# Optimization experiments

Measured on AMD Instinct MI355X. Metric: run time of the kernel, lower is better.

## Reference

```python
import jax, jax.numpy as jnp
import numpy as np

N, E, B = 20000, 160000, 64
NFEAT, NHID, HEADS, NCLASS = 128, 64, 16, 10
GAT_SLOPE = 0.2    # LeakyReLU inside GATv2 attention
OUT_SLOPE = 0.01   # torch.nn.functional.leaky_relu default
TEMPERATURE = 1.0


def _lrelu(x, slope):
    return jnp.where(x >= 0, x, slope * x)


def gatv2_conv(x, src, dst, Wl, bl, Wr, br, att, bias):
    # x: [N, Fin]; PyG GATv2Conv with share_weights=False, concat=False (mean over heads)
    xl = (x @ Wl + bl).reshape(N, HEADS, NHID)   # source-side transform
    xr = (x @ Wr + br).reshape(N, HEADS, NHID)   # target-side transform
    e = _lrelu(xl[src] + xr[dst], GAT_SLOPE)     # [E', H, C] per-edge pre-activation
    logit = jnp.einsum('ehc,hc->eh', e, att)     # [E', H]
    # segment softmax over incoming edges of each target node (self-loops guarantee >=1 edge)
    m = jax.ops.segment_max(logit, dst, num_segments=N)
    m = jnp.where(jnp.isfinite(m), m, 0.0)
    ex = jnp.exp(logit - m[dst])
    den = jax.ops.segment_sum(ex, dst, num_segments=N)
    alpha = ex / den[dst]                        # [E', H]
    out = jax.ops.segment_sum(alpha[:, :, None] * xl[src], dst, num_segments=N)  # [N, H, C]
    return out.mean(axis=1) + bias               # concat=False -> head average, then bias


def setup_inputs() -> dict:
    key = jax.random.key(0)
    ks = jax.random.split(key, 20)
    s = 0.05
    inp = {
        'x': jax.random.normal(ks[0], (N, NFEAT), dtype=jnp.float32),
        'edge_index': jax.random.randint(ks[1], (2, E), 0, N, dtype=jnp.int64)
            if jax.config.jax_enable_x64 else jax.random.randint(ks[1], (2, E), 0, N).astype(jnp.int32),
        'batch': jnp.sort(jax.random.randint(ks[2], (N,), 0, B)).astype(jnp.int32),
        # GATv2 layer 1
        'W1l': jax.random.normal(ks[3], (NFEAT, HEADS * NHID), dtype=jnp.float32) * s,
        'b1l': jnp.zeros((HEADS * NHID,), jnp.float32),
        'W1r': jax.random.normal(ks[4], (NFEAT, HEADS * NHID), dtype=jnp.float32) * s,
        'b1r': jnp.zeros((HEADS * NHID,), jnp.float32),
        'att1': jax.random.normal(ks[5], (HEADS, NHID), dtype=jnp.float32) * s,
        'bias1': jnp.zeros((NHID,), jnp.float32),
        # GATv2 layer 2
        'W2l': jax.random.normal(ks[6], (NHID, HEADS * NHID), dtype=jnp.float32) * s,
        'b2l': jnp.zeros((HEADS * NHID,), jnp.float32),
        'W2r': jax.random.normal(ks[7], (NHID, HEADS * NHID), dtype=jnp.float32) * s,
        'b2r': jnp.zeros((HEADS * NHID,), jnp.float32),
        'att2': jax.random.normal(ks[8], (HEADS, NHID), dtype=jnp.float32) * s,
        'bias2': jnp.zeros((NHID,), jnp.float32),
        # heads
        'Wc': jax.random.normal(ks[9], (NHID, NCLASS), dtype=jnp.float32) * s,
        'bc': jnp.zeros((NCLASS,), jnp.float32),
        'Wv': jax.random.normal(ks[10], (NHID, 1), dtype=jnp.float32) * s,
        'bv': jnp.zeros((1,), jnp.float32),
    }
    return inp


def reference(x, edge_index, batch, W1l, b1l, W1r, b1r, att1, bias1,
              W2l, b2l, W2r, b2r, att2, bias2, Wc, bc, Wv, bv):
    loop = jnp.arange(N, dtype=edge_index.dtype)  # PyG add_self_loops=True
    src = jnp.concatenate([edge_index[0], loop])
    dst = jnp.concatenate([edge_index[1], loop])

    h = _lrelu(gatv2_conv(x, src, dst, W1l, b1l, W1r, b1r, att1, bias1), OUT_SLOPE)
    h = _lrelu(gatv2_conv(h, src, dst, W2l, b2l, W2r, b2r, att2, bias2), OUT_SLOPE)
    # dropout p=0.0 -> identity

    sums = jax.ops.segment_sum(h, batch, num_segments=B)           # [B, NHID]
    cnt = jax.ops.segment_sum(jnp.ones((N,), h.dtype), batch, num_segments=B)
    pooled = sums / jnp.maximum(cnt, 1.0)[:, None]                 # global_mean_pool

    logits = (pooled @ Wc + bc) / TEMPERATURE                      # [B, NCLASS]
    log_var = pooled @ Wv + bv                                     # [B, 1]
    return (logits, log_var)
```

## Files before the change

kernel.cpp:

```cpp
#include <hip/hip_runtime.h>
#include <hip/hip_bf16.h>
#include <hip/hip_fp16.h>
#include <math.h>

#define NN   20000
#define EE   160000
#define NBAT 64
#define NF   128
#define NH   64
#define NHEAD 16
#define NCLS 10
#define ETOT (EE + NN)

typedef __attribute__((ext_vector_type(8))) short short8;
typedef __attribute__((ext_vector_type(8))) _Float16 half8;
typedef __attribute__((ext_vector_type(2))) _Float16 h2v;
typedef __attribute__((ext_vector_type(4))) float f32x4;
typedef unsigned short ushort_t;

#if __has_builtin(__builtin_amdgcn_fdot2)
typedef __fp16 fdot2_t __attribute__((ext_vector_type(2)));
static __device__ __forceinline__ float dot2(h2v a, h2v b, float c) {
    return __builtin_amdgcn_fdot2(__builtin_bit_cast(fdot2_t, a),
                                  __builtin_bit_cast(fdot2_t, b), c, false);
}
#else
static __device__ __forceinline__ float dot2(h2v a, h2v b, float c) {
    return c + (float)a.x * (float)b.x + (float)a.y * (float)b.y;
}
#endif

static __device__ __forceinline__ ushort_t f2bf_rn(float x) {
    unsigned u = __builtin_bit_cast(unsigned, x);
    unsigned r = (u + 0x7fffu + ((u >> 16) & 1u)) >> 16;
    return (ushort_t)r;
}
static __device__ __forceinline__ float bf2f(ushort_t u) {
    unsigned v = (unsigned)u << 16;
    return __builtin_bit_cast(float, v);
}

__global__ void k_hist(const int* __restrict__ ei, int* __restrict__ deg) {
    int e = blockIdx.x * 256 + threadIdx.x;
    if (e < EE) atomicAdd(&deg[ei[EE + e]], 1);
}

__global__ void k_scan(const int* __restrict__ deg, int* __restrict__ rowptr,
                       int* __restrict__ cursor, int* __restrict__ csr) {
    const int T = 1024, PER = (NN + T - 1) / T;
    __shared__ int part[T];
    int t = threadIdx.x;
    int local[PER];
    int s = 0;
    #pragma unroll
    for (int i = 0; i < PER; ++i) {
        int idx = t * PER + i;
        int v = (idx < NN) ? deg[idx] : 0;
        local[i] = v; s += v;
    }
    part[t] = s;
    __syncthreads();
    for (int off = 1; off < T; off <<= 1) {
        int v = (t >= off) ? part[t - off] : 0;
        __syncthreads();
        part[t] += v;
        __syncthreads();
    }
    int ex = (t == 0) ? 0 : part[t - 1];
    #pragma unroll
    for (int i = 0; i < PER; ++i) {
        int idx = t * PER + i;
        if (idx < NN) {
            int base = ex + idx;
            rowptr[idx] = base;
            csr[base]   = idx;
            cursor[idx] = base + 1;
            ex += local[i];
        }
    }
    if (t == T - 1) rowptr[NN] = ex + NN;
}

__global__ void k_scatter(const int* __restrict__ ei, int* __restrict__ cursor,
                          int* __restrict__ csr) {
    int e = blockIdx.x * 256 + threadIdx.x;
    if (e >= EE) return;
    int s = ei[e], d = ei[EE + e];
    int pos = atomicAdd(&cursor[d], 1);
    csr[pos] = s;
}

__global__ void k_bounds(const int* __restrict__ batch, int* __restrict__ bstart) {
    int n = blockIdx.x * 256 + threadIdx.x;
    if (n >= NN) return;
    int b = batch[n];
    if (n == 0) for (int bb = 0; bb <= b; ++bb) bstart[bb] = 0;
    int bn = (n + 1 < NN) ? batch[n + 1] : NBAT;
    for (int bb = b + 1; bb <= bn; ++bb) bstart[bb] = n + 1;
}

__global__ void k_split_w4(
    const float* __restrict__ W0, ushort_t* __restrict__ h0, ushort_t* __restrict__ l0,
    const float* __restrict__ W1, ushort_t* __restrict__ h1, ushort_t* __restrict__ l1,
    const float* __restrict__ W2, ushort_t* __restrict__ h2p, ushort_t* __restrict__ l2,
    const float* __restrict__ W3, ushort_t* __restrict__ h3, ushort_t* __restrict__ l3)
{
    const int z = blockIdx.y;
    const float* W; ushort_t* hi; ushort_t* lo; int K;
    if      (z == 0) { W = W0; hi = h0;  lo = l0; K = NF; }
    else if (z == 1) { W = W1; hi = h1;  lo = l1; K = NF; }
    else if (z == 2) { W = W2; hi = h2p; lo = l2; K = NH; }
    else             { W = W3; hi = h3;  lo = l3; K = NH; }
    int idx = blockIdx.x * 256 + threadIdx.x;
    if (idx >= K * 1024) return;
    int k = idx >> 10, n = idx & 1023;
    float x = W[idx];
    ushort_t h = f2bf_rn(x);
    hi[n * K + k] = h;
    lo[n * K + k] = f2bf_rn(x - bf2f(h));
}


template<int K>
__global__ __launch_bounds__(256) void k_gemm_l1(
    const float* __restrict__ X, int M,
    const ushort_t* __restrict__ W0hi, const ushort_t* __restrict__ W0lo,
    const float* __restrict__ b0, _Float16* __restrict__ O0,
    const ushort_t* __restrict__ W1hi, const ushort_t* __restrict__ W1lo,
    const float* __restrict__ b1, _Float16* __restrict__ O1)
{
    const ushort_t* Whi = blockIdx.z ? W1hi : W0hi;
    const ushort_t* Wlo = blockIdx.z ? W1lo : W0lo;
    const float*    bi  = blockIdx.z ? b1 : b0;
    _Float16*       O   = blockIdx.z ? O1 : O0;

    const int r0 = blockIdx.x * 128;
    const int c0 = blockIdx.y * 128;

    __shared__ __align__(16) ushort_t As_hi[128 * 64];
    __shared__ __align__(16) ushort_t As_lo[128 * 64];
    __shared__ __align__(16) ushort_t Ws_hi[128 * 64];
    __shared__ __align__(16) ushort_t Ws_lo[128 * 64];

    const int t = threadIdx.x;
    const int lane = t & 63;
    const int wv = t >> 6, wr = wv >> 1, wc = wv & 1;
    const int fr = lane & 15;
    const int k0 = (lane >> 4) * 8;

    f32x4 acc[4][4] = {};

    for (int kt = 0; kt < K; kt += 64) {
        #pragma unroll
        for (int p = 0; p < 4; ++p) {
            int idx = p * 256 + t;
            int m  = idx >> 3;
            int kc = (idx & 7) * 8;
            int gr = r0 + m;
            uint4 H = make_uint4(0, 0, 0, 0), L = make_uint4(0, 0, 0, 0);
            if (gr < M) {
                float4 v0 = *(const float4*)(X + (size_t)gr * K + kt + kc);
                float4 v1 = *(const float4*)(X + (size_t)gr * K + kt + kc + 4);
                float vv[8] = {v0.x, v0.y, v0.z, v0.w, v1.x, v1.y, v1.z, v1.w};
                unsigned hh[8], ll[8];
                #pragma unroll
                for (int q = 0; q < 8; ++q) {
                    hh[q] = f2bf_rn(vv[q]);
                    ll[q] = f2bf_rn(vv[q] - bf2f((ushort_t)hh[q]));
                }
                H = make_uint4(hh[0] | (hh[1] << 16), hh[2] | (hh[3] << 16),
                               hh[4] | (hh[5] << 16), hh[6] | (hh[7] << 16));
                L = make_uint4(ll[0] | (ll[1] << 16), ll[2] | (ll[3] << 16),
                               ll[4] | (ll[5] << 16), ll[6] | (ll[7] << 16));
            }
            int sw = (m * 128 + kc * 2) ^ ((m & 7) << 4);
            *(uint4*)((char*)As_hi + sw) = H;
            *(uint4*)((char*)As_lo + sw) = L;
            uint4 wh = *(const uint4*)(Whi + (size_t)(c0 + m) * K + kt + kc);
            uint4 wl = *(const uint4*)(Wlo + (size_t)(c0 + m) * K + kt + kc);
            *(uint4*)((char*)Ws_hi + sw) = wh;
            *(uint4*)((char*)Ws_lo + sw) = wl;
        }
        __syncthreads();

        #pragma unroll
        for (int ks = 0; ks < 64; ks += 32) {
            short8 ah[4], al[4], bh[4], bl[4];
            #pragma unroll
            for (int i = 0; i < 4; ++i) {
                int row = wr * 64 + i * 16 + fr;
                int off = (row * 128 + (ks + k0) * 2) ^ ((row & 7) << 4);
                ah[i] = *(const short8*)((const char*)As_hi + off);
                al[i] = *(const short8*)((const char*)As_lo + off);
            }
            #pragma unroll
            for (int j = 0; j < 4; ++j) {
                int col = wc * 64 + j * 16 + fr;
                int off = (col * 128 + (ks + k0) * 2) ^ ((col & 7) << 4);
                bh[j] = *(const short8*)((const char*)Ws_hi + off);
                bl[j] = *(const short8*)((const char*)Ws_lo + off);
            }
            #pragma unroll
            for (int i = 0; i < 4; ++i)
                #pragma unroll
                for (int j = 0; j < 4; ++j) {
                    acc[i][j] = __builtin_amdgcn_mfma_f32_16x16x32_bf16(ah[i], bh[j], acc[i][j], 0, 0, 0);
                    acc[i][j] = __builtin_amdgcn_mfma_f32_16x16x32_bf16(ah[i], bl[j], acc[i][j], 0, 0, 0);
                    acc[i][j] = __builtin_amdgcn_mfma_f32_16x16x32_bf16(al[i], bh[j], acc[i][j], 0, 0, 0);
                }
        }
        __syncthreads();
    }

    float bj[4];
    #pragma unroll
    for (int j = 0; j < 4; ++j) bj[j] = bi[c0 + wc * 64 + j * 16 + fr];
    #pragma unroll
    for (int i = 0; i < 4; ++i) {
        int rbase = r0 + wr * 64 + i * 16 + (lane >> 4) * 4;
        #pragma unroll
        for (int r = 0; r < 4; ++r) {
            int gr = rbase + r;
            if (gr < M) {
                #pragma unroll
                for (int j = 0; j < 4; ++j)
                    O[(size_t)gr * 1024 + c0 + wc * 64 + j * 16 + fr] =
                        (_Float16)(acc[i][j][r] + bj[j]);
            }
        }
    }
}

template<int K>
__global__ __launch_bounds__(256) void k_gemm_mfma(
    const ushort_t* __restrict__ Ahi, const ushort_t* __restrict__ Alo, int M,
    const ushort_t* __restrict__ W0hi, const ushort_t* __restrict__ W0lo,
    const float* __restrict__ b0, _Float16* __restrict__ O0,
    const ushort_t* __restrict__ W1hi, const ushort_t* __restrict__ W1lo,
    const float* __restrict__ b1, _Float16* __restrict__ O1)
{
    const ushort_t* Whi = blockIdx.z ? W1hi : W0hi;
    const ushort_t* Wlo = blockIdx.z ? W1lo : W0lo;
    const float*    bi  = blockIdx.z ? b1 : b0;
    _Float16*       O   = blockIdx.z ? O1 : O0;

    const int r0 = blockIdx.x * 128;
    const int c0 = blockIdx.y * 128;

    __shared__ __align__(16) ushort_t As_hi[128 * 64];
    __shared__ __align__(16) ushort_t As_lo[128 * 64];
    __shared__ __align__(16) ushort_t Ws_hi[128 * 64];
    __shared__ __align__(16) ushort_t Ws_lo[128 * 64];

    const int t = threadIdx.x;
    const int lane = t & 63;
    const int wv = t >> 6, wr = wv >> 1, wc = wv & 1;
    const int fr = lane & 15;
    const int k0 = (lane >> 4) * 8;

    f32x4 acc[4][4] = {};

    for (int kt = 0; kt < K; kt += 64) {
        #pragma unroll
        for (int p = 0; p < 4; ++p) {
            int idx = p * 256 + t;
            int m  = idx >> 3;
            int kc = (idx & 7) * 8;
            int gr = r0 + m;
            uint4 vh = make_uint4(0, 0, 0, 0), vl = make_uint4(0, 0, 0, 0);
            if (gr < M) {
                vh = *(const uint4*)(Ahi + (size_t)gr * K + kt + kc);
                vl = *(const uint4*)(Alo + (size_t)gr * K + kt + kc);
            }
            int sw = (m * 128 + kc * 2) ^ ((m & 7) << 4);
            *(uint4*)((char*)As_hi + sw) = vh;
            *(uint4*)((char*)As_lo + sw) = vl;
            uint4 wh = *(const uint4*)(Whi + (size_t)(c0 + m) * K + kt + kc);
            uint4 wl = *(const uint4*)(Wlo + (size_t)(c0 + m) * K + kt + kc);
            *(uint4*)((char*)Ws_hi + sw) = wh;
            *(uint4*)((char*)Ws_lo + sw) = wl;
        }
        __syncthreads();

        #pragma unroll
        for (int ks = 0; ks < 64; ks += 32) {
            short8 ah[4], al[4], bh[4], bl[4];
            #pragma unroll
            for (int i = 0; i < 4; ++i) {
                int row = wr * 64 + i * 16 + fr;
                int off = (row * 128 + (ks + k0) * 2) ^ ((row & 7) << 4);
                ah[i] = *(const short8*)((const char*)As_hi + off);
                al[i] = *(const short8*)((const char*)As_lo + off);
            }
            #pragma unroll
            for (int j = 0; j < 4; ++j) {
                int col = wc * 64 + j * 16 + fr;
                int off = (col * 128 + (ks + k0) * 2) ^ ((col & 7) << 4);
                bh[j] = *(const short8*)((const char*)Ws_hi + off);
                bl[j] = *(const short8*)((const char*)Ws_lo + off);
            }
            #pragma unroll
            for (int i = 0; i < 4; ++i)
                #pragma unroll
                for (int j = 0; j < 4; ++j) {
                    acc[i][j] = __builtin_amdgcn_mfma_f32_16x16x32_bf16(ah[i], bh[j], acc[i][j], 0, 0, 0);
                    acc[i][j] = __builtin_amdgcn_mfma_f32_16x16x32_bf16(ah[i], bl[j], acc[i][j], 0, 0, 0);
                    acc[i][j] = __builtin_amdgcn_mfma_f32_16x16x32_bf16(al[i], bh[j], acc[i][j], 0, 0, 0);
                }
        }
        __syncthreads();
    }

    float bj[4];
    #pragma unroll
    for (int j = 0; j < 4; ++j) bj[j] = bi[c0 + wc * 64 + j * 16 + fr];
    #pragma unroll
    for (int i = 0; i < 4; ++i) {
        int rbase = r0 + wr * 64 + i * 16 + (lane >> 4) * 4;
        #pragma unroll
        for (int r = 0; r < 4; ++r) {
            int gr = rbase + r;
            if (gr < M) {
                #pragma unroll
                for (int j = 0; j < 4; ++j)
                    O[(size_t)gr * 1024 + c0 + wc * 64 + j * 16 + fr] =
                        (_Float16)(acc[i][j][r] + bj[j]);
            }
        }
    }
}

static __device__ __forceinline__ float logit8(
    half8 a0, half8 a1, half8 xr0, half8 xr1, const h2v* att2)
{
    half8 t0 = a0 + xr0;
    half8 t1 = a1 + xr1;
    t0 = __builtin_elementwise_max(t0, t0 * (_Float16)0.2f);
    t1 = __builtin_elementwise_max(t1, t1 * (_Float16)0.2f);
    const h2v* p0 = (const h2v*)&t0;
    const h2v* p1 = (const h2v*)&t1;
    float lg = 0.f;
    #pragma unroll
    for (int j = 0; j < 4; ++j) lg = dot2(p0[j], att2[j], lg);
    #pragma unroll
    for (int j = 0; j < 4; ++j) lg = dot2(p1[j], att2[4 + j], lg);
    return lg;
}

template<int SPLIT>
__global__ __launch_bounds__(256) void k_attn(
    const _Float16* __restrict__ xl, const _Float16* __restrict__ xr,
    const float* __restrict__ att, const float* __restrict__ bias,
    const int* __restrict__ rowptr, const int* __restrict__ csr,
    float* __restrict__ hout, ushort_t* __restrict__ hhi, ushort_t* __restrict__ hlo)
{
    const int wave = threadIdx.x >> 6;
    const int lane = threadIdx.x & 63;
    const int n = blockIdx.x * 4 + wave;
    if (n >= NN) return;
    const int h  = lane >> 2;
    const int cc = lane & 3;
    const int cb = h * NH + cc * 16;

    h2v att2[8];
    #pragma unroll
    for (int i = 0; i < 4; ++i) {
        float4 a = *(const float4*)(att + cb + i * 4);
        att2[i * 2 + 0] = h2v{(_Float16)a.x, (_Float16)a.y};
        att2[i * 2 + 1] = h2v{(_Float16)a.z, (_Float16)a.w};
    }
    const half8 xr0 = *(const half8*)(xr + (size_t)n * 1024 + cb);
    const half8 xr1 = *(const half8*)(xr + (size_t)n * 1024 + cb + 8);

    float acc[16];
    #pragma unroll
    for (int j = 0; j < 16; ++j) acc[j] = 0.f;
    float den = 0.f;

    const int e0 = rowptr[n], e1 = rowptr[n + 1];
    for (int e = e0; e < e1; e += 4) {
        int src[4];
        #pragma unroll
        for (int j = 0; j < 4; ++j) {
            int ee = e + j;
            src[j] = csr[(ee < e1) ? ee : (e1 - 1)];
        }
        half8 xa0[4], xa1[4];
        #pragma unroll
        for (int j = 0; j < 4; ++j) {
            const _Float16* p = xl + (size_t)src[j] * 1024 + cb;
            xa0[j] = *(const half8*)p;
            xa1[j] = *(const half8*)(p + 8);
        }
        #pragma unroll
        for (int j = 0; j < 4; ++j) {
            float lg = logit8(xa0[j], xa1[j], xr0, xr1, att2);
            lg += __shfl_xor(lg, 1);
            lg += __shfl_xor(lg, 2);
            float p = (e + j < e1) ? __expf(lg) : 0.f;
            den += p;
            const _Float16* va = (const _Float16*)&xa0[j];
            const _Float16* vb = (const _Float16*)&xa1[j];
            #pragma unroll
            for (int q = 0; q < 8; ++q) acc[q]     = fmaf((float)va[q], p, acc[q]);
            #pragma unroll
            for (int q = 0; q < 8; ++q) acc[8 + q] = fmaf((float)vb[q], p, acc[8 + q]);
        }
    }

    const float inv = 1.f / den;
    float v[16];
    #pragma unroll
    for (int j = 0; j < 16; ++j) v[j] = acc[j] * inv;
    #pragma unroll
    for (int mask = 4; mask <= 32; mask <<= 1)
        #pragma unroll
        for (int j = 0; j < 16; ++j) v[j] += __shfl_xor(v[j], mask);

    if (h == 0) {
        float bvv[16];
        #pragma unroll
        for (int i = 0; i < 4; ++i)
            *(float4*)(bvv + i * 4) = *(const float4*)(bias + cc * 16 + i * 4);
        #pragma unroll
        for (int i = 0; i < 4; ++i) {
            float o[4];
            #pragma unroll
            for (int r = 0; r < 4; ++r) {
                float tt = v[i * 4 + r] * 0.0625f + bvv[i * 4 + r];
                o[r] = fmaxf(tt, 0.01f * tt);
            }
            if (SPLIT) {
                ushort4 hh, ll;
                hh.x = f2bf_rn(o[0]); ll.x = f2bf_rn(o[0] - bf2f(hh.x));
                hh.y = f2bf_rn(o[1]); ll.y = f2bf_rn(o[1] - bf2f(hh.y));
                hh.z = f2bf_rn(o[2]); ll.z = f2bf_rn(o[2] - bf2f(hh.z));
                hh.w = f2bf_rn(o[3]); ll.w = f2bf_rn(o[3] - bf2f(hh.w));
                *(ushort4*)(hhi + (size_t)n * NH + cc * 16 + i * 4) = hh;
                *(ushort4*)(hlo + (size_t)n * NH + cc * 16 + i * 4) = ll;
            } else {
                *(float4*)(hout + (size_t)n * NH + cc * 16 + i * 4) =
                    make_float4(o[0], o[1], o[2], o[3]);
            }
        }
    }
}

#define PNODES 128
__global__ __launch_bounds__(256) void k_pool_partial(
    const float* __restrict__ h2buf, const int* __restrict__ batch,
    float* __restrict__ sums)
{
    const int n0 = blockIdx.x * PNODES;
    const int c = threadIdx.x & 63;
    const int r = threadIdx.x >> 6;
    const int nend = (n0 + PNODES < NN) ? n0 + PNODES : NN;
    float s = 0.f;
    int bcur = -1;
    for (int n = n0 + r; n < nend; n += 4) {
        int b = batch[n];
        if (b != bcur) {
            if (bcur >= 0) atomicAdd(&sums[bcur * NH + c], s);
            bcur = b; s = 0.f;
        }
        s += h2buf[(size_t)n * NH + c];
    }
    if (bcur >= 0) atomicAdd(&sums[bcur * NH + c], s);
}

__global__ void k_heads(const float* __restrict__ sums, const int* __restrict__ bstart,
                        const float* __restrict__ Wc, const float* __restrict__ bc,
                        const float* __restrict__ Wv, const float* __restrict__ bv,
                        float* __restrict__ out)
{
    const int b = blockIdx.x, c = threadIdx.x;
    const float cnt = (float)(bstart[b + 1] - bstart[b]);
    const float pooled = sums[b * NH + c] / fmaxf(cnt, 1.f);
    __shared__ float pl[NH];
    pl[c] = pooled;
    __syncthreads();
    if (c < NCLS) {
        float a = bc[c];
        for (int k = 0; k < NH; ++k) a = fmaf(pl[k], Wc[k * NCLS + c], a);
        out[b * NCLS + c] = a;
    } else if (c == NCLS) {
        float a = bv[0];
        for (int k = 0; k < NH; ++k) a = fmaf(pl[k], Wv[k], a);
        out[NBAT * NCLS + b] = a;
    }
}

extern "C" void kernel_launch(void* const* d_in, const int* in_sizes, int n_in,
                              void* d_out, int out_size, void* d_ws, size_t ws_size,
                              hipStream_t stream)
{
    const float* x     = (const float*)d_in[0];
    const int*   ei    = (const int*)  d_in[1];
    const int*   batch = (const int*)  d_in[2];
    const float* W1l = (const float*)d_in[3],  *b1l = (const float*)d_in[4];
    const float* W1r = (const float*)d_in[5],  *b1r = (const float*)d_in[6];
    const float* att1 = (const float*)d_in[7], *bias1 = (const float*)d_in[8];
    const float* W2l = (const float*)d_in[9],  *b2l = (const float*)d_in[10];
    const float* W2r = (const float*)d_in[11], *b2r = (const float*)d_in[12];
    const float* att2 = (const float*)d_in[13], *bias2 = (const float*)d_in[14];
    const float* Wc = (const float*)d_in[15],  *bc = (const float*)d_in[16];
    const float* Wv = (const float*)d_in[17],  *bv = (const float*)d_in[18];
    float* out = (float*)d_out;

    char* ws = (char*)d_ws;
    size_t off = 0;
    auto carve = [&](size_t bytes) {
        char* p = ws + off;
        off = (off + bytes + 255) & ~(size_t)255;
        return p;
    };
    _Float16* xl    = (_Float16*)carve((size_t)NN * 1024 * 2);
    _Float16* xr    = (_Float16*)carve((size_t)NN * 1024 * 2);
    float*    h2b   = (float*)carve((size_t)NN * NH * 4);
    float*    psums = (float*)carve((size_t)NBAT * NH * 4);
    ushort_t* h1hi  = (ushort_t*)carve((size_t)NN * NH * 2);
    ushort_t* h1lo  = (ushort_t*)carve((size_t)NN * NH * 2);
    ushort_t* Wt1lh = (ushort_t*)carve((size_t)1024 * NF * 2);
    ushort_t* Wt1ll = (ushort_t*)carve((size_t)1024 * NF * 2);
    ushort_t* Wt1rh = (ushort_t*)carve((size_t)1024 * NF * 2);
    ushort_t* Wt1rl = (ushort_t*)carve((size_t)1024 * NF * 2);
    ushort_t* Wt2lh = (ushort_t*)carve((size_t)1024 * NH * 2);
    ushort_t* Wt2ll = (ushort_t*)carve((size_t)1024 * NH * 2);
    ushort_t* Wt2rh = (ushort_t*)carve((size_t)1024 * NH * 2);
    ushort_t* Wt2rl = (ushort_t*)carve((size_t)1024 * NH * 2);
    int*      deg    = (int*)carve((size_t)NN * 4);
    int*      cursor = (int*)carve((size_t)NN * 4);
    int*      rowptr = (int*)carve((size_t)(NN + 1) * 4);
    int*      csr    = (int*)carve((size_t)ETOT * 4);
    int*      bstart = (int*)carve((size_t)(NBAT + 1) * 4);

    hipMemsetAsync(deg, 0, (size_t)NN * 4, stream);
    k_hist   <<<(EE + 255) / 256, 256, 0, stream>>>(ei, deg);
    k_scan   <<<1, 1024, 0, stream>>>(deg, rowptr, cursor, csr);
    k_scatter<<<(EE + 255) / 256, 256, 0, stream>>>(ei, cursor, csr);
    k_bounds <<<(NN + 255) / 256, 256, 0, stream>>>(batch, bstart);

    k_split_w4<<<dim3((NF * 1024 + 255) / 256, 4), 256, 0, stream>>>(
        W1l, Wt1lh, Wt1ll, W1r, Wt1rh, Wt1rl,
        W2l, Wt2lh, Wt2ll, W2r, Wt2rh, Wt2rl);

    const int MB = (NN + 127) / 128;
    k_gemm_l1<NF><<<dim3(MB, 8, 2), 256, 0, stream>>>(
        x, NN, Wt1lh, Wt1ll, b1l, xl, Wt1rh, Wt1rl, b1r, xr);
    k_attn<1><<<NN / 4, 256, 0, stream>>>(xl, xr, att1, bias1, rowptr, csr,
                                          (float*)nullptr, h1hi, h1lo);
    k_gemm_mfma<NH><<<dim3(MB, 8, 2), 256, 0, stream>>>(
        h1hi, h1lo, NN, Wt2lh, Wt2ll, b2l, xl, Wt2rh, Wt2rl, b2r, xr);
    k_attn<0><<<NN / 4, 256, 0, stream>>>(xl, xr, att2, bias2, rowptr, csr,
                                          h2b, (ushort_t*)nullptr, (ushort_t*)nullptr);
    hipMemsetAsync(psums, 0, (size_t)NBAT * NH * 4, stream);
    k_pool_partial<<<(NN + PNODES - 1) / PNODES, 256, 0, stream>>>(h2b, batch, psums);
    k_heads<<<NBAT, NH, 0, stream>>>(psums, bstart, Wc, bc, Wv, bv, out);
}
```

Baseline: 386.0 us.

## Replace split-bf16 triple MFMA GEMMs with single fp16 MFMA and staged stores

Drops the hi/lo bf16 split emulation of fp32 in both projection GEMMs, using plain fp16 operands and one f16 MFMA per tile instead of three. This also halves the weight and activation staging traffic and the LDS footprint. Layer-2 input h1 is now stored as fp16, and the layer-2 GEMM loses its K loop since K fits in a single tile. Outputs are staged through swizzled LDS so global writes become coalesced 16-byte stores. The cost is lower precision: fp16 operands have a 10-bit mantissa instead of the near-fp32 accuracy of the split, which may affect tolerance.

```diff
diff --git a/kernel.cpp b/kernel.cpp
--- a/kernel.cpp
+++ b/kernel.cpp
@@ -12,7 +12,6 @@
 #define NCLS 10
 #define ETOT (EE + NN)
 
-typedef __attribute__((ext_vector_type(8))) short short8;
 typedef __attribute__((ext_vector_type(8))) _Float16 half8;
 typedef __attribute__((ext_vector_type(2))) _Float16 h2v;
 typedef __attribute__((ext_vector_type(4))) float f32x4;
@@ -29,16 +28,6 @@
     return c + (float)a.x * (float)b.x + (float)a.y * (float)b.y;
 }
 #endif
-
-static __device__ __forceinline__ ushort_t f2bf_rn(float x) {
-    unsigned u = __builtin_bit_cast(unsigned, x);
-    unsigned r = (u + 0x7fffu + ((u >> 16) & 1u)) >> 16;
-    return (ushort_t)r;
-}
-static __device__ __forceinline__ float bf2f(ushort_t u) {
-    unsigned v = (unsigned)u << 16;
-    return __builtin_bit_cast(float, v);
-}
 
 __global__ void k_hist(const int* __restrict__ ei, int* __restrict__ deg) {
     int e = blockIdx.x * 256 + threadIdx.x;
@@ -100,47 +89,40 @@
 }
 
 __global__ void k_split_w4(
-    const float* __restrict__ W0, ushort_t* __restrict__ h0, ushort_t* __restrict__ l0,
-    const float* __restrict__ W1, ushort_t* __restrict__ h1, ushort_t* __restrict__ l1,
-    const float* __restrict__ W2, ushort_t* __restrict__ h2p, ushort_t* __restrict__ l2,
-    const float* __restrict__ W3, ushort_t* __restrict__ h3, ushort_t* __restrict__ l3)
+    const float* __restrict__ W0, _Float16* __restrict__ T0,
+    const float* __restrict__ W1, _Float16* __restrict__ T1,
+    const float* __restrict__ W2, _Float16* __restrict__ T2,
+    const float* __restrict__ W3, _Float16* __restrict__ T3)
 {
     const int z = blockIdx.y;
-    const float* W; ushort_t* hi; ushort_t* lo; int K;
-    if      (z == 0) { W = W0; hi = h0;  lo = l0; K = NF; }
-    else if (z == 1) { W = W1; hi = h1;  lo = l1; K = NF; }
-    else if (z == 2) { W = W2; hi = h2p; lo = l2; K = NH; }
-    else             { W = W3; hi = h3;  lo = l3; K = NH; }
+    const float* W; _Float16* T; int K;
+    if      (z == 0) { W = W0; T = T0; K = NF; }
+    else if (z == 1) { W = W1; T = T1; K = NF; }
+    else if (z == 2) { W = W2; T = T2; K = NH; }
+    else             { W = W3; T = T3; K = NH; }
     int idx = blockIdx.x * 256 + threadIdx.x;
     if (idx >= K * 1024) return;
     int k = idx >> 10, n = idx & 1023;
-    float x = W[idx];
-    ushort_t h = f2bf_rn(x);
-    hi[n * K + k] = h;
-    lo[n * K + k] = f2bf_rn(x - bf2f(h));
+    T[n * K + k] = (_Float16)W[idx];
 }
 
 
 template<int K>
 __global__ __launch_bounds__(256) void k_gemm_l1(
     const float* __restrict__ X, int M,
-    const ushort_t* __restrict__ W0hi, const ushort_t* __restrict__ W0lo,
-    const float* __restrict__ b0, _Float16* __restrict__ O0,
-    const ushort_t* __restrict__ W1hi, const ushort_t* __restrict__ W1lo,
-    const float* __restrict__ b1, _Float16* __restrict__ O1)
-{
-    const ushort_t* Whi = blockIdx.z ? W1hi : W0hi;
-    const ushort_t* Wlo = blockIdx.z ? W1lo : W0lo;
-    const float*    bi  = blockIdx.z ? b1 : b0;
-    _Float16*       O   = blockIdx.z ? O1 : O0;
+    const _Float16* __restrict__ Wt0, const float* __restrict__ b0, _Float16* __restrict__ O0,
+    const _Float16* __restrict__ Wt1, const float* __restrict__ b1, _Float16* __restrict__ O1)
+{
+    const _Float16* Wt = blockIdx.z ? Wt1 : Wt0;
+    const float*    bi = blockIdx.z ? b1 : b0;
+    _Float16*       O  = blockIdx.z ? O1 : O0;
 
     const int r0 = blockIdx.x * 128;
     const int c0 = blockIdx.y * 128;
 
-    __shared__ __align__(16) ushort_t As_hi[128 * 64];
-    __shared__ __align__(16) ushort_t As_lo[128 * 64];
-    __shared__ __align__(16) ushort_t Ws_hi[128 * 64];
-    __shared__ __align__(16) ushort_t Ws_lo[128 * 64];
+    __shared__ __align__(16) ushort_t SH[128 * 128];
+    char* AsB = (char*)SH;
+    char* WsB = (char*)SH + 16384;
 
     const int t = threadIdx.x;
     const int lane = t & 63;
@@ -157,57 +139,42 @@
             int m  = idx >> 3;
             int kc = (idx & 7) * 8;
             int gr = r0 + m;
-            uint4 H = make_uint4(0, 0, 0, 0), L = make_uint4(0, 0, 0, 0);
+            half8 hv = {};
             if (gr < M) {
                 float4 v0 = *(const float4*)(X + (size_t)gr * K + kt + kc);
                 float4 v1 = *(const float4*)(X + (size_t)gr * K + kt + kc + 4);
-                float vv[8] = {v0.x, v0.y, v0.z, v0.w, v1.x, v1.y, v1.z, v1.w};
-                unsigned hh[8], ll[8];
-                #pragma unroll
-                for (int q = 0; q < 8; ++q) {
-                    hh[q] = f2bf_rn(vv[q]);
-                    ll[q] = f2bf_rn(vv[q] - bf2f((ushort_t)hh[q]));
-                }
-                H = make_uint4(hh[0] | (hh[1] << 16), hh[2] | (hh[3] << 16),
-                               hh[4] | (hh[5] << 16), hh[6] | (hh[7] << 16));
-                L = make_uint4(ll[0] | (ll[1] << 16), ll[2] | (ll[3] << 16),
-                               ll[4] | (ll[5] << 16), ll[6] | (ll[7] << 16));
+                hv[0] = (_Float16)v0.x; hv[1] = (_Float16)v0.y;
+                hv[2] = (_Float16)v0.z; hv[3] = (_Float16)v0.w;
+                hv[4] = (_Float16)v1.x; hv[5] = (_Float16)v1.y;
+                hv[6] = (_Float16)v1.z; hv[7] = (_Float16)v1.w;
             }
             int sw = (m * 128 + kc * 2) ^ ((m & 7) << 4);
-            *(uint4*)((char*)As_hi + sw) = H;
-            *(uint4*)((char*)As_lo + sw) = L;
-            uint4 wh = *(const uint4*)(Whi + (size_t)(c0 + m) * K + kt + kc);
-            uint4 wl = *(const uint4*)(Wlo + (size_t)(c0 + m) * K + kt + kc);
-            *(uint4*)((char*)Ws_hi + sw) = wh;
-            *(uint4*)((char*)Ws_lo + sw) = wl;
+            *(uint4*)(AsB + sw) = __builtin_bit_cast(uint4, hv);
+            uint4 wv4 = *(const uint4*)(Wt + (size_t)(c0 + m) * K + kt + kc);
+            *(uint4*)(WsB + sw) = wv4;
         }
         __syncthreads();
 
         #pragma unroll
         for (int ks = 0; ks < 64; ks += 32) {
-            short8 ah[4], al[4], bh[4], bl[4];
+            half8 a[4], b[4];
             #pragma unroll
             for (int i = 0; i < 4; ++i) {
                 int row = wr * 64 + i * 16 + fr;
                 int off = (row * 128 + (ks + k0) * 2) ^ ((row & 7) << 4);
-                ah[i] = *(const short8*)((const char*)As_hi + off);
-                al[i] = *(const short8*)((const char*)As_lo + off);
+                a[i] = *(const half8*)(AsB + off);
             }
             #pragma unroll
             for (int j = 0; j < 4; ++j) {
                 int col = wc * 64 + j * 16 + fr;
                 int off = (col * 128 + (ks + k0) * 2) ^ ((col & 7) << 4);
-                bh[j] = *(const short8*)((const char*)Ws_hi + off);
-                bl[j] = *(const short8*)((const char*)Ws_lo + off);
+                b[j] = *(const half8*)(WsB + off);
             }
             #pragma unroll
             for (int i = 0; i < 4; ++i)
                 #pragma unroll
-                for (int j = 0; j < 4; ++j) {
-                    acc[i][j] = __builtin_amdgcn_mfma_f32_16x16x32_bf16(ah[i], bh[j], acc[i][j], 0, 0, 0);
-                    acc[i][j] = __builtin_amdgcn_mfma_f32_16x16x32_bf16(ah[i], bl[j], acc[i][j], 0, 0, 0);
-                    acc[i][j] = __builtin_amdgcn_mfma_f32_16x16x32_bf16(al[i], bh[j], acc[i][j], 0, 0, 0);
-                }
+                for (int j = 0; j < 4; ++j)
+                    acc[i][j] = __builtin_amdgcn_mfma_f32_16x16x32_f16(a[i], b[j], acc[i][j], 0, 0, 0);
         }
         __syncthreads();
     }
@@ -217,40 +184,48 @@
     for (int j = 0; j < 4; ++j) bj[j] = bi[c0 + wc * 64 + j * 16 + fr];
     #pragma unroll
     for (int i = 0; i < 4; ++i) {
-        int rbase = r0 + wr * 64 + i * 16 + (lane >> 4) * 4;
         #pragma unroll
         for (int r = 0; r < 4; ++r) {
-            int gr = rbase + r;
-            if (gr < M) {
-                #pragma unroll
-                for (int j = 0; j < 4; ++j)
-                    O[(size_t)gr * 1024 + c0 + wc * 64 + j * 16 + fr] =
-                        (_Float16)(acc[i][j][r] + bj[j]);
+            int row_l = wr * 64 + i * 16 + (lane >> 4) * 4 + r;
+            int s = ((row_l >> 2) & 7) << 4;
+            #pragma unroll
+            for (int j = 0; j < 4; ++j) {
+                int col_l = wc * 64 + j * 16 + fr;
+                *(_Float16*)((char*)SH + ((row_l * 256 + col_l * 2) ^ s)) =
+                    (_Float16)(acc[i][j][r] + bj[j]);
             }
         }
     }
+    __syncthreads();
+    #pragma unroll
+    for (int it = 0; it < 8; ++it) {
+        int idx = it * 256 + t;
+        int row_l = idx >> 4, c16 = idx & 15;
+        int gr = r0 + row_l;
+        if (gr < M) {
+            int s = ((row_l >> 2) & 7) << 4;
+            uint4 v = *(const uint4*)((char*)SH + ((row_l * 256 + c16 * 16) ^ s));
+            *(uint4*)(O + (size_t)gr * 1024 + c0 + c16 * 8) = v;
+        }
+    }
 }
 
 template<int K>
-__global__ __launch_bounds__(256) void k_gemm_mfma(
-    const ushort_t* __restrict__ Ahi, const ushort_t* __restrict__ Alo, int M,
-    const ushort_t* __restrict__ W0hi, const ushort_t* __restrict__ W0lo,
-    const float* __restrict__ b0, _Float16* __restrict__ O0,
-    const ushort_t* __restrict__ W1hi, const ushort_t* __restrict__ W1lo,
-    const float* __restrict__ b1, _Float16* __restrict__ O1)
-{
-    const ushort_t* Whi = blockIdx.z ? W1hi : W0hi;
-    const ushort_t* Wlo = blockIdx.z ? W1lo : W0lo;
-    const float*    bi  = blockIdx.z ? b1 : b0;
-    _Float16*       O   = blockIdx.z ? O1 : O0;
+__global__ __launch_bounds__(256) void k_gemm_l2(
+    const _Float16* __restrict__ A, int M,
+    const _Float16* __restrict__ Wt0, const float* __restrict__ b0, _Float16* __restrict__ O0,
+    const _Float16* __restrict__ Wt1, const float* __restrict__ b1, _Float16* __restrict__ O1)
+{
+    const _Float16* Wt = blockIdx.z ? Wt1 : Wt0;
+    const float*    bi = blockIdx.z ? b1 : b0;
+    _Float16*       O  = blockIdx.z ? O1 : O0;
 
     const int r0 = blockIdx.x * 128;
     const int c0 = blockIdx.y * 128;
 
-    __shared__ __align__(16) ushort_t As_hi[128 * 64];
-    __shared__ __align__(16) ushort_t As_lo[128 * 64];
-    __shared__ __align__(16) ushort_t Ws_hi[128 * 64];
-    __shared__ __align__(16) ushort_t Ws_lo[128 * 64];
+    __shared__ __align__(16) ushort_t SH[128 * 128];
+    char* AsB = (char*)SH;
+    char* WsB = (char*)SH + 16384;
 
     const int t = threadIdx.x;
     const int lane = t & 63;
@@ -260,72 +235,71 @@
 
     f32x4 acc[4][4] = {};
 
-    for (int kt = 0; kt < K; kt += 64) {
-        #pragma unroll
-        for (int p = 0; p < 4; ++p) {
-            int idx = p * 256 + t;
-            int m  = idx >> 3;
-            int kc = (idx & 7) * 8;
-            int gr = r0 + m;
-            uint4 vh = make_uint4(0, 0, 0, 0), vl = make_uint4(0, 0, 0, 0);
-            if (gr < M) {
-                vh = *(const uint4*)(Ahi + (size_t)gr * K + kt + kc);
-                vl = *(const uint4*)(Alo + (size_t)gr * K + kt + kc);
+    #pragma unroll
+    for (int p = 0; p < 4; ++p) {
+        int idx = p * 256 + t;
+        int m  = idx >> 3;
+        int kc = (idx & 7) * 8;
+        int gr = r0 + m;
+        uint4 av = make_uint4(0, 0, 0, 0);
+        if (gr < M) av = *(const uint4*)(A + (size_t)gr * K + kc);
+        int sw = (m * 128 + kc * 2) ^ ((m & 7) << 4);
+        *(uint4*)(AsB + sw) = av;
+        uint4 wv4 = *(const uint4*)(Wt + (size_t)(c0 + m) * K + kc);
+        *(uint4*)(WsB + sw) = wv4;
+    }
+    __syncthreads();
+
+    #pragma unroll
+    for (int ks = 0; ks < 64; ks += 32) {
+        half8 a[4], b[4];
+        #pragma unroll
+        for (int i = 0; i < 4; ++i) {
+            int row = wr * 64 + i * 16 + fr;
+            int off = (row * 128 + (ks + k0) * 2) ^ ((row & 7) << 4);
+            a[i] = *(const half8*)(AsB + off);
+        }
+        #pragma unroll
+        for (int j = 0; j < 4; ++j) {
+            int col = wc * 64 + j * 16 + fr;
+            int off = (col * 128 + (ks + k0) * 2) ^ ((col & 7) << 4);
+            b[j] = *(const half8*)(WsB + off);
+        }
+        #pragma unroll
+        for (int i = 0; i < 4; ++i)
+            #pragma unroll
+            for (int j = 0; j < 4; ++j)
+                acc[i][j] = __builtin_amdgcn_mfma_f32_16x16x32_f16(a[i], b[j], acc[i][j], 0, 0, 0);
+    }
+    __syncthreads();
+
+    float bj[4];
+    #pragma unroll
+    for (int j = 0; j < 4; ++j) bj[j] = bi[c0 + wc * 64 + j * 16 + fr];
+    #pragma unroll
+    for (int i = 0; i < 4; ++i) {
+        #pragma unroll
+        for (int r = 0; r < 4; ++r) {
+            int row_l = wr * 64 + i * 16 + (lane >> 4) * 4 + r;
+            int s = ((row_l >> 2) & 7) << 4;
+            #pragma unroll
+            for (int j = 0; j < 4; ++j) {
+                int col_l = wc * 64 + j * 16 + fr;
+                *(_Float16*)((char*)SH + ((row_l * 256 + col_l * 2) ^ s)) =
+                    (_Float16)(acc[i][j][r] + bj[j]);
             }
-            int sw = (m * 128 + kc * 2) ^ ((m & 7) << 4);
-            *(uint4*)((char*)As_hi + sw) = vh;
-            *(uint4*)((char*)As_lo + sw) = vl;
-            uint4 wh = *(const uint4*)(Whi + (size_t)(c0 + m) * K + kt + kc);
-            uint4 wl = *(const uint4*)(Wlo + (size_t)(c0 + m) * K + kt + kc);
-            *(uint4*)((char*)Ws_hi + sw) = wh;
-            *(uint4*)((char*)Ws_lo + sw) = wl;
-        }
-        __syncthreads();
-
-        #pragma unroll
-        for (int ks = 0; ks < 64; ks += 32) {
-            short8 ah[4], al[4], bh[4], bl[4];
-            #pragma unroll
-            for (int i = 0; i < 4; ++i) {
-                int row = wr * 64 + i * 16 + fr;
-                int off = (row * 128 + (ks + k0) * 2) ^ ((row & 7) << 4);
-                ah[i] = *(const short8*)((const char*)As_hi + off);
-                al[i] = *(const short8*)((const char*)As_lo + off);
-            }
-            #pragma unroll
-            for (int j = 0; j < 4; ++j) {
-                int col = wc * 64 + j * 16 + fr;
-                int off = (col * 128 + (ks + k0) * 2) ^ ((col & 7) << 4);
-                bh[j] = *(const short8*)((const char*)Ws_hi + off);
-                bl[j] = *(const short8*)((const char*)Ws_lo + off);
-            }
-            #pragma unroll
-            for (int i = 0; i < 4; ++i)
-                #pragma unroll
-                for (int j = 0; j < 4; ++j) {
-                    acc[i][j] = __builtin_amdgcn_mfma_f32_16x16x32_bf16(ah[i], bh[j], acc[i][j], 0, 0, 0);
-                    acc[i][j] = __builtin_amdgcn_mfma_f32_16x16x32_bf16(ah[i], bl[j], acc[i][j], 0, 0, 0);
-                    acc[i][j] = __builtin_amdgcn_mfma_f32_16x16x32_bf16(al[i], bh[j], acc[i][j], 0, 0, 0);
-                }
-        }
-        __syncthreads();
-    }
-
-    float bj[4];
-    #pragma unroll
-    for (int j = 0; j < 4; ++j) bj[j] = bi[c0 + wc * 64 + j * 16 + fr];
-    #pragma unroll
-    for (int i = 0; i < 4; ++i) {
-        int rbase = r0 + wr * 64 + i * 16 + (lane >> 4) * 4;
-        #pragma unroll
-        for (int r = 0; r < 4; ++r) {
-            int gr = rbase + r;
-            if (gr < M) {
-                #pragma unroll
-                for (int j = 0; j < 4; ++j)
-                    O[(size_t)gr * 1024 + c0 + wc * 64 + j * 16 + fr] =
-                        (_Float16)(acc[i][j][r] + bj[j]);
-            }
+        }
+    }
+    __syncthreads();
+    #pragma unroll
+    for (int it = 0; it < 8; ++it) {
+        int idx = it * 256 + t;
+        int row_l = idx >> 4, c16 = idx & 15;
+        int gr = r0 + row_l;
+        if (gr < M) {
+            int s = ((row_l >> 2) & 7) << 4;
+            uint4 v = *(const uint4*)((char*)SH + ((row_l * 256 + c16 * 16) ^ s));
+            *(uint4*)(O + (size_t)gr * 1024 + c0 + c16 * 8) = v;
         }
     }
 }
@@ -352,7 +326,7 @@
     const _Float16* __restrict__ xl, const _Float16* __restrict__ xr,
     const float* __restrict__ att, const float* __restrict__ bias,
     const int* __restrict__ rowptr, const int* __restrict__ csr,
-    float* __restrict__ hout, ushort_t* __restrict__ hhi, ushort_t* __restrict__ hlo)
+    float* __restrict__ hout, _Float16* __restrict__ h1out)
 {
     const int wave = threadIdx.x >> 6;
     const int lane = threadIdx.x & 63;
@@ -422,26 +396,23 @@
         #pragma unroll
         for (int i = 0; i < 4; ++i)
             *(float4*)(bvv + i * 4) = *(const float4*)(bias + cc * 16 + i * 4);
-        #pragma unroll
-        for (int i = 0; i < 4; ++i) {
-            float o[4];
-            #pragma unroll
-            for (int r = 0; r < 4; ++r) {
-                float tt = v[i * 4 + r] * 0.0625f + bvv[i * 4 + r];
-                o[r] = fmaxf(tt, 0.01f * tt);
-            }
-            if (SPLIT) {
-                ushort4 hh, ll;
-                hh.x = f2bf_rn(o[0]); ll.x = f2bf_rn(o[0] - bf2f(hh.x));
-                hh.y = f2bf_rn(o[1]); ll.y = f2bf_rn(o[1] - bf2f(hh.y));
-                hh.z = f2bf_rn(o[2]); ll.z = f2bf_rn(o[2] - bf2f(hh.z));
-                hh.w = f2bf_rn(o[3]); ll.w = f2bf_rn(o[3] - bf2f(hh.w));
-                *(ushort4*)(hhi + (size_t)n * NH + cc * 16 + i * 4) = hh;
-                *(ushort4*)(hlo + (size_t)n * NH + cc * 16 + i * 4) = ll;
-            } else {
+        float o[16];
+        #pragma unroll
+        for (int j = 0; j < 16; ++j) {
+            float tt = v[j] * 0.0625f + bvv[j];
+            o[j] = fmaxf(tt, 0.01f * tt);
+        }
+        if (SPLIT) {
+            half8 o0, o1;
+            #pragma unroll
+            for (int j = 0; j < 8; ++j) { o0[j] = (_Float16)o[j]; o1[j] = (_Float16)o[8 + j]; }
+            *(half8*)(h1out + (size_t)n * NH + cc * 16)     = o0;
+            *(half8*)(h1out + (size_t)n * NH + cc * 16 + 8) = o1;
+        } else {
+            #pragma unroll
+            for (int i = 0; i < 4; ++i)
                 *(float4*)(hout + (size_t)n * NH + cc * 16 + i * 4) =
-                    make_float4(o[0], o[1], o[2], o[3]);
-            }
+                    make_float4(o[i * 4], o[i * 4 + 1], o[i * 4 + 2], o[i * 4 + 3]);
         }
     }
 }
@@ -518,16 +489,11 @@
     _Float16* xr    = (_Float16*)carve((size_t)NN * 1024 * 2);
     float*    h2b   = (float*)carve((size_t)NN * NH * 4);
     float*    psums = (float*)carve((size_t)NBAT * NH * 4);
-    ushort_t* h1hi  = (ushort_t*)carve((size_t)NN * NH * 2);
-    ushort_t* h1lo  = (ushort_t*)carve((size_t)NN * NH * 2);
-    ushort_t* Wt1lh = (ushort_t*)carve((size_t)1024 * NF * 2);
-    ushort_t* Wt1ll = (ushort_t*)carve((size_t)1024 * NF * 2);
-    ushort_t* Wt1rh = (ushort_t*)carve((size_t)1024 * NF * 2);
-    ushort_t* Wt1rl = (ushort_t*)carve((size_t)1024 * NF * 2);
-    ushort_t* Wt2lh = (ushort_t*)carve((size_t)1024 * NH * 2);
-    ushort_t* Wt2ll = (ushort_t*)carve((size_t)1024 * NH * 2);
-    ushort_t* Wt2rh = (ushort_t*)carve((size_t)1024 * NH * 2);
-    ushort_t* Wt2rl = (ushort_t*)carve((size_t)1024 * NH * 2);
+    _Float16* h1    = (_Float16*)carve((size_t)NN * NH * 2);
+    _Float16* Wt1l  = (_Float16*)carve((size_t)1024 * NF * 2);
+    _Float16* Wt1r  = (_Float16*)carve((size_t)1024 * NF * 2);
+    _Float16* Wt2l  = (_Float16*)carve((size_t)1024 * NH * 2);
+    _Float16* Wt2r  = (_Float16*)carve((size_t)1024 * NH * 2);
     int*      deg    = (int*)carve((size_t)NN * 4);
     int*      cursor = (int*)carve((size_t)NN * 4);
     int*      rowptr = (int*)carve((size_t)(NN + 1) * 4);
@@ -541,18 +507,17 @@
     k_bounds <<<(NN + 255) / 256, 256, 0, stream>>>(batch, bstart);
 
     k_split_w4<<<dim3((NF * 1024 + 255) / 256, 4), 256, 0, stream>>>(
-        W1l, Wt1lh, Wt1ll, W1r, Wt1rh, Wt1rl,
-        W2l, Wt2lh, Wt2ll, W2r, Wt2rh, Wt2rl);
+        W1l, Wt1l, W1r, Wt1r, W2l, Wt2l, W2r, Wt2r);
 
     const int MB = (NN + 127) / 128;
     k_gemm_l1<NF><<<dim3(MB, 8, 2), 256, 0, stream>>>(
-        x, NN, Wt1lh, Wt1ll, b1l, xl, Wt1rh, Wt1rl, b1r, xr);
+        x, NN, Wt1l, b1l, xl, Wt1r, b1r, xr);
     k_attn<1><<<NN / 4, 256, 0, stream>>>(xl, xr, att1, bias1, rowptr, csr,
-                                          (float*)nullptr, h1hi, h1lo);
-    k_gemm_mfma<NH><<<dim3(MB, 8, 2), 256, 0, stream>>>(
-        h1hi, h1lo, NN, Wt2lh, Wt2ll, b2l, xl, Wt2rh, Wt2rl, b2r, xr);
+                                          (float*)nullptr, h1);
+    k_gemm_l2<NH><<<dim3(MB, 8, 2), 256, 0, stream>>>(
+        h1, NN, Wt2l, b2l, xl, Wt2r, b2r, xr);
     k_attn<0><<<NN / 4, 256, 0, stream>>>(xl, xr, att2, bias2, rowptr, csr,
-                                          h2b, (ushort_t*)nullptr, (ushort_t*)nullptr);
+                                          h2b, (_Float16*)nullptr);
     hipMemsetAsync(psums, 0, (size_t)NBAT * NH * 4, stream);
     k_pool_partial<<<(NN + PNODES - 1) / PNODES, 256, 0, stream>>>(h2b, batch, psums);
     k_heads<<<NBAT, NH, 0, stream>>>(psums, bstart, Wc, bc, Wv, bv, out);
```

Measured after the change: 357.4 us. -7.4%, faster.
